# Kernel optimization log

Hardware: AMD Instinct MI355X
Metric: run time of the kernel (lower is better)

The kernel has to match this reference:

```python
import jax, jax.numpy as jnp
import numpy as np

ENC_DIM, DEC_DIM, ATT_DIM = 2048, 512, 512
B, P = 256, 196


def setup_inputs() -> dict:
    key = jax.random.key(0)
    ks = jax.random.split(key, 8)
    s_e = 1.0 / np.sqrt(ENC_DIM)
    s_d = 1.0 / np.sqrt(DEC_DIM)
    s_a = 1.0 / np.sqrt(ATT_DIM)
    return {
        "enc_feature": jax.random.normal(ks[0], (B, P, ENC_DIM), jnp.float32),
        "dec_hidden": jax.random.normal(ks[1], (B, DEC_DIM), jnp.float32),
        "W_enc": jax.random.uniform(ks[2], (ATT_DIM, ENC_DIM), jnp.float32, -s_e, s_e),
        "b_enc": jax.random.uniform(ks[3], (ATT_DIM,), jnp.float32, -s_e, s_e),
        "W_dec": jax.random.uniform(ks[4], (ATT_DIM, DEC_DIM), jnp.float32, -s_d, s_d),
        "b_dec": jax.random.uniform(ks[5], (ATT_DIM,), jnp.float32, -s_d, s_d),
        "W_full": jax.random.uniform(ks[6], (1, ATT_DIM), jnp.float32, -s_a, s_a),
        "b_full": jax.random.uniform(ks[7], (1,), jnp.float32, -s_a, s_a),
    }


def reference(enc_feature, dec_hidden, W_enc, b_enc, W_dec, b_dec, W_full, b_full):
    # att1: [B, P, A]; att2: [B, A]
    att1 = jnp.einsum('bpe,ae->bpa', enc_feature, W_enc) + b_enc
    att2 = jnp.einsum('bd,ad->ba', dec_hidden, W_dec) + b_dec
    h = jax.nn.relu(att1 + att2[:, None, :])            # [B, P, A]
    att = jnp.einsum('bpa,a->bp', h, W_full[0]) + b_full[0]  # [B, P]
    alpha = jax.nn.softmax(att, axis=1)                 # softmax over pixels
    atten_w_enc = jnp.einsum('bpe,bp->be', enc_feature, alpha)
    return atten_w_enc, alpha
```

## Files before the change

kernel.cpp:

```cpp
#include <hip/hip_runtime.h>
#include <hip/hip_bf16.h>
#include <stdint.h>

#define ENC_DIM 2048
#define DEC_DIM 512
#define ATT_DIM 512
#define BATCH   256
#define PIX     196
#define M_TOTAL (BATCH*PIX)
#define NT      (ENC_DIM/64)

typedef unsigned short u16;
typedef __attribute__((ext_vector_type(8))) short  bf16x8;
typedef __attribute__((ext_vector_type(4))) float  f32x4;

__device__ __forceinline__ void gll16(const void* g, void* l) {
    __builtin_amdgcn_global_load_lds(
        (const __attribute__((address_space(1))) unsigned int*)g,
        (__attribute__((address_space(3))) unsigned int*)l,
        16, 0, 0);
}

union Pack8 {
    uint4 u;
    __hip_bfloat16 h[8];
};

__device__ __forceinline__ uint4 cvt8(float4 a, float4 b) {
    Pack8 p;
    p.h[0] = __float2bfloat16(a.x); p.h[1] = __float2bfloat16(a.y);
    p.h[2] = __float2bfloat16(a.z); p.h[3] = __float2bfloat16(a.w);
    p.h[4] = __float2bfloat16(b.x); p.h[5] = __float2bfloat16(b.y);
    p.h[6] = __float2bfloat16(b.z); p.h[7] = __float2bfloat16(b.w);
    return p.u;
}

__global__ void k_convert(const float* __restrict__ W, u16* __restrict__ Wb) {
    int idx = blockIdx.x * 256 + threadIdx.x;
    const float4* s = (const float4*)W + (size_t)idx * 2;
    ((uint4*)Wb)[idx] = cvt8(s[0], s[1]);
}

__global__ void k_att2(const float* __restrict__ dec, const float* __restrict__ Wd,
                       const float* __restrict__ b_enc, const float* __restrict__ b_dec,
                       float* __restrict__ att2f) {
    int b = blockIdx.x;
    int t = threadIdx.x;
    __shared__ float dec_s[DEC_DIM];
    ((float2*)dec_s)[t] = ((const float2*)(dec + (size_t)b * DEC_DIM))[t];
    __syncthreads();
    #pragma unroll
    for (int rep = 0; rep < 2; ++rep) {
        int a = t + rep * 256;
        const float4* w = (const float4*)(Wd + (size_t)a * DEC_DIM);
        float acc = 0.f;
        #pragma unroll 4
        for (int e = 0; e < DEC_DIM / 4; ++e) {
            float4 wv = w[e];
            float4 dv = ((const float4*)dec_s)[e];
            acc += wv.x * dv.x + wv.y * dv.y + wv.z * dv.z + wv.w * dv.w;
        }
        att2f[(size_t)b * ATT_DIM + a] = acc + b_enc[a] + b_dec[a];
    }
}


#define FENCE  asm volatile("" ::: "memory")
#define LGKM0  asm volatile("s_waitcnt lgkmcnt(0)" ::: "memory")
#define VMC(N) asm volatile("s_waitcnt vmcnt(" #N ")" ::: "memory")
#define SBARF  do { FENCE; __builtin_amdgcn_s_barrier(); FENCE; } while (0)

#define ISSUE_A(KT, F) do { const float* _p = a_src + (size_t)(KT) * 64;               \
    F[0] = *(const float4*)(_p);                                                       \
    F[1] = *(const float4*)(_p + 4);                                                   \
    F[2] = *(const float4*)(_p + (size_t)64 * ENC_DIM);                                \
    F[3] = *(const float4*)(_p + (size_t)64 * ENC_DIM + 4); } while (0)

#define WRITE_A(Q, F) do {                                                             \
    *(uint4*)(&As[Q][aw_off])        = cvt8(F[0], F[1]);                               \
    *(uint4*)(&As[Q][aw_off + 4096]) = cvt8(F[2], F[3]); } while (0)

#define STAGE_B(KT, Q) do { const u16* _b = b_src + (size_t)(KT) * 64;                 \
    _Pragma("unroll") for (int s = 0; s < 8; ++s)                                      \
        gll16(_b + (size_t)s * 64 * ENC_DIM, &Bs[Q][s * 4096 + b_dst]); } while (0)

#define COMPUTE(P) do {                                                                \
    _Pragma("unroll") for (int ks = 0; ks < 2; ++ks) {                                 \
        const int _axo = ks ? axo1 : axo0;                                             \
        bf16x8 af[4], bf[8];                                                           \
        _Pragma("unroll") for (int m = 0; m < 4; ++m)                                  \
            af[m] = *(const bf16x8*)(&As[P][a_row_off + m * 1024 + _axo]);             \
        _Pragma("unroll") for (int n = 0; n < 8; ++n)                                  \
            bf[n] = *(const bf16x8*)(&Bs[P][b_row_off + n * 1024 + _axo]);             \
        __builtin_amdgcn_s_setprio(1);                                                 \
        _Pragma("unroll") for (int m = 0; m < 4; ++m)                                  \
            _Pragma("unroll") for (int n = 0; n < 8; ++n)                              \
                acc[m][n] = __builtin_amdgcn_mfma_f32_16x16x32_bf16(af[m], bf[n], acc[m][n], 0, 0, 0); \
        __builtin_amdgcn_s_setprio(0);                                                 \
    } } while (0)

__global__ void __launch_bounds__(512, 1)
k_gemm(const float* __restrict__ enc, const u16* __restrict__ Wb,
       const float* __restrict__ att2f, const float* __restrict__ Wfull,
       float* __restrict__ att_part) {
    const int mb = blockIdx.x;
    const int t  = threadIdx.x;
    const int lane = t & 63, wave = t >> 6;
    const int wm = wave >> 2, wn = wave & 3;
    const int fr = lane & 15, fq = lane >> 4;

    __shared__ u16 As[2][128 * 64];
    __shared__ u16 Bs[2][512 * 64];

    f32x4 acc[4][8];
    #pragma unroll
    for (int m = 0; m < 4; ++m)
        #pragma unroll
        for (int n = 0; n < 8; ++n)
            acc[m][n] = (f32x4){0.f, 0.f, 0.f, 0.f};

    const int arow  = t >> 3;
    const int aslot = t & 7;
    const float* a_src = enc + (size_t)(mb * 128 + arow) * ENC_DIM + aslot * 8;
    const int aw_off = arow * 64 + ((aslot ^ (arow & 7))) * 8;

    const int brl = lane >> 3, bslot = lane & 7;
    const u16* b_src = Wb + (size_t)(wave * 8 + brl) * ENC_DIM + ((bslot ^ brl)) * 8;
    const int b_dst = (wave * 8) * 64;

    const int r7 = fr & 7;
    const int axo0 = ((fq    ) ^ r7) * 8;
    const int axo1 = ((fq | 4) ^ r7) * 8;
    const int a_row_off = (wm * 64 + fr) * 64;
    const int b_row_off = (wn * 128 + fr) * 64;

    float4 eE[4], eO[4];

    ISSUE_A(0, eE); FENCE;
    STAGE_B(0, 0);
    WRITE_A(0, eE);
    FENCE; ISSUE_A(1, eO);
    FENCE; ISSUE_A(2, eE);
    VMC(8);
    LGKM0;
    SBARF;

    for (int kt = 0; kt < NT - 4; kt += 2) {
        WRITE_A(1, eO);
        STAGE_B(kt + 1, 1); FENCE;
        ISSUE_A(kt + 3, eO);
        COMPUTE(0);
        VMC(4);
        LGKM0;
        SBARF;
        WRITE_A(0, eE);
        STAGE_B(kt + 2, 0); FENCE;
        ISSUE_A(kt + 4, eE);
        COMPUTE(1);
        VMC(4);
        LGKM0;
        SBARF;
    }

    {
        WRITE_A(1, eO);
        STAGE_B(29, 1); FENCE;
        ISSUE_A(31, eO);
        COMPUTE(0);
        VMC(4);
        LGKM0;
        SBARF;
    }
    {
        WRITE_A(0, eE);
        STAGE_B(30, 0);
        COMPUTE(1);
        VMC(0);
        LGKM0;
        SBARF;
    }
    {
        WRITE_A(1, eO);
        STAGE_B(31, 1);
        COMPUTE(0);
        VMC(0);
        LGKM0;
        SBARF;
    }
    COMPUTE(1);

    const int row_base = mb * 128 + wm * 64 + fq * 4;
    const int col_base = wn * 128 + fr;
    float wf[8];
    #pragma unroll
    for (int n = 0; n < 8; ++n) wf[n] = Wfull[col_base + n * 16];

    #pragma unroll
    for (int m = 0; m < 4; ++m) {
        #pragma unroll
        for (int r = 0; r < 4; ++r) {
            const int grow = row_base + m * 16 + r;
            const int bidx = grow / PIX;
            const float* a2 = att2f + (size_t)bidx * ATT_DIM;
            float ssum = 0.f;
            #pragma unroll
            for (int n = 0; n < 8; ++n) {
                float v = acc[m][n][r] + a2[col_base + n * 16];
                v = fmaxf(v, 0.f);
                ssum += v * wf[n];
            }
            #pragma unroll
            for (int off = 1; off < 16; off <<= 1)
                ssum += __shfl_xor(ssum, off, 64);
            if (fr == 0)
                att_part[(size_t)wn * M_TOTAL + grow] = ssum;
        }
    }
}

__global__ void k_soft(const float* __restrict__ att_part, const float* __restrict__ enc,
                       float* __restrict__ out) {
    const int b  = blockIdx.x >> 1;
    const int ec = blockIdx.x & 1;
    const int t  = threadIdx.x;
    __shared__ float red[256];
    __shared__ float alpha_s[PIX];

    float myatt = -1e30f;
    if (t < PIX) {
        float s = 0.f;
        #pragma unroll
        for (int j = 0; j < 4; ++j) s += att_part[(size_t)j * M_TOTAL + b * PIX + t];
        myatt = s;
    }
    red[t] = myatt;
    __syncthreads();
    for (int o = 128; o > 0; o >>= 1) {
        if (t < o) red[t] = fmaxf(red[t], red[t + o]);
        __syncthreads();
    }
    const float mx = red[0];
    __syncthreads();
    float e = 0.f;
    if (t < PIX) e = __expf(myatt - mx);
    red[t] = e;
    __syncthreads();
    for (int o = 128; o > 0; o >>= 1) {
        if (t < o) red[t] += red[t + o];
        __syncthreads();
    }
    const float inv = 1.f / red[0];
    if (t < PIX) {
        float al = e * inv;
        alpha_s[t] = al;
        if (ec == 0) out[(size_t)BATCH * ENC_DIM + b * PIX + t] = al;
    }
    __syncthreads();

    float4 acc = {0.f, 0.f, 0.f, 0.f};
    const float* ebase = enc + (size_t)b * PIX * ENC_DIM + ec * 1024 + t * 4;
    #pragma unroll 4
    for (int p = 0; p < PIX; ++p) {
        float4 x = *(const float4*)(ebase + (size_t)p * ENC_DIM);
        float a = alpha_s[p];
        acc.x += a * x.x; acc.y += a * x.y; acc.z += a * x.z; acc.w += a * x.w;
    }
    *(float4*)(out + (size_t)b * ENC_DIM + ec * 1024 + t * 4) = acc;
}

extern "C" void kernel_launch(void* const* d_in, const int* in_sizes, int n_in,
                              void* d_out, int out_size, void* d_ws, size_t ws_size,
                              hipStream_t stream) {
    const float* enc    = (const float*)d_in[0];
    const float* dec    = (const float*)d_in[1];
    const float* W_enc  = (const float*)d_in[2];
    const float* b_enc  = (const float*)d_in[3];
    const float* W_dec  = (const float*)d_in[4];
    const float* b_dec  = (const float*)d_in[5];
    const float* W_full = (const float*)d_in[6];

    char* ws = (char*)d_ws;
    u16*   Wb    = (u16*)ws;
    float* att2f = (float*)(ws + 2 * 1024 * 1024);
    float* att_p = (float*)(ws + 2 * 1024 * 1024 + 512 * 1024);

    hipLaunchKernelGGL(k_convert, dim3(512), dim3(256), 0, stream, W_enc, Wb);
    hipLaunchKernelGGL(k_att2,    dim3(256), dim3(256), 0, stream, dec, W_dec, b_enc, b_dec, att2f);
    hipLaunchKernelGGL(k_gemm,    dim3(392), dim3(512), 0, stream, enc, Wb, att2f, W_full, att_p);
    hipLaunchKernelGGL(k_soft,    dim3(512), dim3(256), 0, stream, att_p, enc, (float*)d_out);
}
```

Baseline: 263.0 us.

## Fuse softmax and attention-weighted sum into GEMM epilogue with split-partial combine

Measured after the change: 282.8 us. +7.5%, slower.

```diff
diff --git a/kernel.cpp b/kernel.cpp
--- a/kernel.cpp
+++ b/kernel.cpp
@@ -102,7 +102,8 @@
 __global__ void __launch_bounds__(512, 1)
 k_gemm(const float* __restrict__ enc, const u16* __restrict__ Wb,
        const float* __restrict__ att2f, const float* __restrict__ Wfull,
-       float* __restrict__ att_part) {
+       float* __restrict__ exp_att, float* __restrict__ part_vec,
+       float* __restrict__ part_sum) {
     const int mb = blockIdx.x;
     const int t  = threadIdx.x;
     const int lane = t & 63, wave = t >> 6;
@@ -189,8 +190,9 @@
     }
     COMPUTE(1);
 
-    const int row_base = mb * 128 + wm * 64 + fq * 4;
+    float* lds_f = (float*)&As[0][0];
     const int col_base = wn * 128 + fr;
+    const int rloc = wm * 64 + fq * 4;
     float wf[8];
     #pragma unroll
     for (int n = 0; n < 8; ++n) wf[n] = Wfull[col_base + n * 16];
@@ -199,9 +201,8 @@
     for (int m = 0; m < 4; ++m) {
         #pragma unroll
         for (int r = 0; r < 4; ++r) {
-            const int grow = row_base + m * 16 + r;
-            const int bidx = grow / PIX;
-            const float* a2 = att2f + (size_t)bidx * ATT_DIM;
+            const int grow = mb * 128 + rloc + m * 16 + r;
+            const float* a2 = att2f + (size_t)(grow / PIX) * ATT_DIM;
             float ssum = 0.f;
             #pragma unroll
             for (int n = 0; n < 8; ++n) {
@@ -213,59 +214,75 @@
             for (int off = 1; off < 16; off <<= 1)
                 ssum += __shfl_xor(ssum, off, 64);
             if (fr == 0)
-                att_part[(size_t)wn * M_TOTAL + grow] = ssum;
+                lds_f[wn * 128 + rloc + m * 16 + r] = ssum;
         }
     }
-}
-
-__global__ void k_soft(const float* __restrict__ att_part, const float* __restrict__ enc,
-                       float* __restrict__ out) {
-    const int b  = blockIdx.x >> 1;
-    const int ec = blockIdx.x & 1;
-    const int t  = threadIdx.x;
-    __shared__ float red[256];
-    __shared__ float alpha_s[PIX];
-
-    float myatt = -1e30f;
-    if (t < PIX) {
+    SBARF;
+
+    const int b0    = (128 * mb) / PIX;
+    const int split = min(128, PIX * (b0 + 1) - 128 * mb);
+    if (t < 128) {
+        float a = lds_f[t] + lds_f[128 + t] + lds_f[256 + t] + lds_f[384 + t];
+        float e = __expf(a);
+        lds_f[512 + t] = e;
+        exp_att[(size_t)mb * 128 + t] = e;
+    }
+    SBARF;
+    if (t < 2) {
+        const int lo = t ? split : 0, hi = t ? 128 : split;
         float s = 0.f;
-        #pragma unroll
-        for (int j = 0; j < 4; ++j) s += att_part[(size_t)j * M_TOTAL + b * PIX + t];
-        myatt = s;
-    }
-    red[t] = myatt;
-    __syncthreads();
-    for (int o = 128; o > 0; o >>= 1) {
-        if (t < o) red[t] = fmaxf(red[t], red[t + o]);
-        __syncthreads();
-    }
-    const float mx = red[0];
-    __syncthreads();
-    float e = 0.f;
-    if (t < PIX) e = __expf(myatt - mx);
-    red[t] = e;
-    __syncthreads();
-    for (int o = 128; o > 0; o >>= 1) {
-        if (t < o) red[t] += red[t + o];
-        __syncthreads();
-    }
-    const float inv = 1.f / red[0];
-    if (t < PIX) {
-        float al = e * inv;
-        alpha_s[t] = al;
-        if (ec == 0) out[(size_t)BATCH * ENC_DIM + b * PIX + t] = al;
-    }
-    __syncthreads();
-
-    float4 acc = {0.f, 0.f, 0.f, 0.f};
-    const float* ebase = enc + (size_t)b * PIX * ENC_DIM + ec * 1024 + t * 4;
-    #pragma unroll 4
-    for (int p = 0; p < PIX; ++p) {
-        float4 x = *(const float4*)(ebase + (size_t)p * ENC_DIM);
-        float a = alpha_s[p];
-        acc.x += a * x.x; acc.y += a * x.y; acc.z += a * x.z; acc.w += a * x.w;
-    }
-    *(float4*)(out + (size_t)b * ENC_DIM + ec * 1024 + t * 4) = acc;
+        for (int r = lo; r < hi; ++r) s += lds_f[512 + r];
+        part_sum[mb * 2 + t] = s;
+    }
+
+    const float* erow = enc + (size_t)(mb * 128) * ENC_DIM + t * 4;
+    float4 s0 = {0.f, 0.f, 0.f, 0.f}, s1 = {0.f, 0.f, 0.f, 0.f};
+    for (int r = 0; r < split; ++r) {
+        float e = lds_f[512 + r];
+        float4 x = *(const float4*)(erow + (size_t)r * ENC_DIM);
+        s0.x += e * x.x; s0.y += e * x.y; s0.z += e * x.z; s0.w += e * x.w;
+    }
+    for (int r = split; r < 128; ++r) {
+        float e = lds_f[512 + r];
+        float4 x = *(const float4*)(erow + (size_t)r * ENC_DIM);
+        s1.x += e * x.x; s1.y += e * x.y; s1.z += e * x.z; s1.w += e * x.w;
+    }
+    *(float4*)&part_vec[((size_t)mb * 2 + 0) * ENC_DIM + t * 4] = s0;
+    *(float4*)&part_vec[((size_t)mb * 2 + 1) * ENC_DIM + t * 4] = s1;
+}
+
+__global__ void k_combine(const float* __restrict__ exp_att,
+                          const float* __restrict__ part_vec,
+                          const float* __restrict__ part_sum,
+                          float* __restrict__ out) {
+    const int b = blockIdx.x;
+    const int t = threadIdx.x;
+    const int row0 = b * PIX;
+    const int mb_lo = row0 >> 7;
+    const int mb_hi = (row0 + PIX - 1) >> 7;
+
+    float Z = 0.f;
+    for (int mb = mb_lo; mb <= mb_hi; ++mb) {
+        int seg = b - ((mb << 7) / PIX);
+        if (seg >= 0 && seg < 2) Z += part_sum[mb * 2 + seg];
+    }
+    const float invZ = 1.f / Z;
+
+    #pragma unroll
+    for (int c = 0; c < 2; ++c) {
+        const int e0 = t * 8 + c * 4;
+        float4 s = {0.f, 0.f, 0.f, 0.f};
+        for (int mb = mb_lo; mb <= mb_hi; ++mb) {
+            int seg = b - ((mb << 7) / PIX);
+            if (seg < 0 || seg > 1) continue;
+            float4 v = *(const float4*)&part_vec[((size_t)mb * 2 + seg) * ENC_DIM + e0];
+            s.x += v.x; s.y += v.y; s.z += v.z; s.w += v.w;
+        }
+        s.x *= invZ; s.y *= invZ; s.z *= invZ; s.w *= invZ;
+        *(float4*)&out[(size_t)b * ENC_DIM + e0] = s;
+    }
+    if (t < PIX)
+        out[(size_t)BATCH * ENC_DIM + row0 + t] = exp_att[row0 + t] * invZ;
 }
 
 extern "C" void kernel_launch(void* const* d_in, const int* in_sizes, int n_in,
@@ -280,12 +297,16 @@
     const float* W_full = (const float*)d_in[6];
 
     char* ws = (char*)d_ws;
-    u16*   Wb    = (u16*)ws;
-    float* att2f = (float*)(ws + 2 * 1024 * 1024);
-    float* att_p = (float*)(ws + 2 * 1024 * 1024 + 512 * 1024);
+    u16*   Wb       = (u16*)ws;
+    float* att2f    = (float*)(ws + 2097152);
+    float* exp_att  = (float*)(ws + 2621440);
+    float* part_sum = (float*)(ws + 2883584);
+    float* part_vec = (float*)(ws + 2887680);
 
     hipLaunchKernelGGL(k_convert, dim3(512), dim3(256), 0, stream, W_enc, Wb);
     hipLaunchKernelGGL(k_att2,    dim3(256), dim3(256), 0, stream, dec, W_dec, b_enc, b_dec, att2f);
-    hipLaunchKernelGGL(k_gemm,    dim3(392), dim3(512), 0, stream, enc, Wb, att2f, W_full, att_p);
-    hipLaunchKernelGGL(k_soft,    dim3(512), dim3(256), 0, stream, att_p, enc, (float*)d_out);
-}
+    hipLaunchKernelGGL(k_gemm,    dim3(392), dim3(512), 0, stream, enc, Wb, att2f, W_full,
+                       exp_att, part_vec, part_sum);
+    hipLaunchKernelGGL(k_combine, dim3(256), dim3(256), 0, stream, exp_att, part_vec, part_sum,
+                       (float*)d_out);
+}
```
